# Optimization experiments

Measured on AMD Instinct MI355X. Metric: run time of the kernel, lower is better.

Reference implementation:

```python
import jax, jax.numpy as jnp
import numpy as np

N = 50000   # nodes
E = 800000  # edges (avg degree 16)
D = 128     # in_dim == out_dim
EPS = 1e-5  # LayerNorm eps (torch default)


def setup_inputs() -> dict:
    key = jax.random.key(0)
    ks = jax.random.split(key, 8)
    x = jax.random.normal(ks[0], (N, D), dtype=jnp.float32)
    edge_row = jax.random.randint(ks[1], (E,), 0, N, dtype=jnp.int32)
    edge_col = jax.random.randint(ks[2], (E,), 0, N, dtype=jnp.int32)
    edge_val = jax.random.uniform(ks[3], (E,), dtype=jnp.float32)
    W = jax.random.normal(ks[4], (D, D), dtype=jnp.float32) / np.sqrt(D).astype(np.float32)
    b = jnp.zeros((D,), jnp.float32)
    gamma = jnp.ones((D,), jnp.float32)
    beta = jnp.zeros((D,), jnp.float32)
    return {"x": x, "edge_val": edge_val, "W": W, "b": b,
            "gamma": gamma, "beta": beta,
            "edge_row": edge_row, "edge_col": edge_col}


def reference(x, edge_val, W, b, gamma, beta, edge_row, edge_col):
    # SpMM: support = adj @ x, adj in COO form (row, col, val)
    msgs = edge_val[:, None] * x[edge_col]                      # [E, D] gather
    support = jax.ops.segment_sum(msgs, edge_row, num_segments=x.shape[0])  # [N, D]
    # Linear (torch stores weight as [out, in])
    h = support @ W.T + b                                       # [N, D]
    # LayerNorm over last dim
    mu = jnp.mean(h, axis=-1, keepdims=True)
    var = jnp.mean(jnp.square(h - mu), axis=-1, keepdims=True)
    h = (h - mu) * jax.lax.rsqrt(var + EPS) * gamma + beta
    # ReLU; dropout is identity at inference
    return jax.nn.relu(h)
```

## Files before the change

### kernel.cpp

```cpp
#include <hip/hip_runtime.h>

#define D 128
#define LN_EPS 1e-5f
#define RPB 16
#define POISON 0xAAAAAAAAu
#define BINSTRIDE 4864
#define SBF_STRIDE 68
#define SH_STRIDE 132
#define ECAP 68
#define EMAX 64
#define P1BLOCKS 512
#define P1THREADS 1024
#define DENSECAP 1600
#define CURSTRIDE 16

typedef __attribute__((ext_vector_type(8))) short short8;
typedef __attribute__((ext_vector_type(4))) float f32x4;

union FragU { uint4 u; short8 s; };

__device__ __forceinline__ unsigned bf16_hi(float f) {
    unsigned u = __float_as_uint(f);
    return (u + 0x7FFFu + ((u >> 16) & 1u)) & 0xFFFF0000u;
}
__device__ __forceinline__ float lo16f(unsigned u) { return __uint_as_float(u << 16); }
__device__ __forceinline__ float hi16f(unsigned u) { return __uint_as_float(u & 0xFFFF0000u); }

__global__ void __launch_bounds__(P1THREADS) prep1_kernel(
    const int* __restrict__ edge_row, const int* __restrict__ edge_col,
    const float* __restrict__ edge_val,
    const float* __restrict__ W, const float* __restrict__ x,
    unsigned* __restrict__ Wb, unsigned* __restrict__ xb16,
    unsigned* __restrict__ bin_cursor, uint2* __restrict__ binbuf,
    int E, int n8, int nbins, int epb) {
    __shared__ int cntL[256];
    __shared__ int curL[256];
    __shared__ int lbaseL[256];
    __shared__ int gbaseL[256];
    __shared__ int tmp[2][256];
    __shared__ uint2 dense[DENSECAP];
    int t = threadIdx.x;
    int gid = blockIdx.x * P1THREADS + t;
    int gsz = gridDim.x * P1THREADS;

    if (t < 256) cntL[t] = 0;

    if (gid < 8192) {
        int u  = gid & 3;
        int L  = (gid >> 2) & 63;
        int nt = (gid >> 8) & 7;
        int kt = gid >> 11;
        int n = nt * 16 + (L & 15);
        int k = kt * 32 + (L >> 4) * 8 + u * 2;
        unsigned lo = bf16_hi(W[n * D + k]) >> 16;
        unsigned hi = bf16_hi(W[n * D + k + 1]);
        Wb[gid] = hi | lo;
    }

    for (int j = gid; j < n8; j += gsz) {
        float4 a = *(const float4*)(x + (size_t)j * 8);
        float4 c = *(const float4*)(x + (size_t)j * 8 + 4);
        uint4 o;
        o.x = bf16_hi(a.y) | (bf16_hi(a.x) >> 16);
        o.y = bf16_hi(a.w) | (bf16_hi(a.z) >> 16);
        o.z = bf16_hi(c.y) | (bf16_hi(c.x) >> 16);
        o.w = bf16_hi(c.w) | (bf16_hi(c.z) >> 16);
        *(uint4*)(xb16 + (size_t)j * 4) = o;
    }
    __syncthreads();

    int e0 = blockIdx.x * epb;
    int e1 = e0 + epb; if (e1 > E) e1 = E;
    int nume = e1 - e0; if (nume < 0) nume = 0;

    {
        int i = e0 + t * 4;
        for (; i + 3 < e1; i += P1THREADS * 4) {
            int4 r = *(const int4*)(edge_row + i);
            atomicAdd(&cntL[r.x >> 8], 1);
            atomicAdd(&cntL[r.y >> 8], 1);
            atomicAdd(&cntL[r.z >> 8], 1);
            atomicAdd(&cntL[r.w >> 8], 1);
        }
        for (; i < e1; ++i) atomicAdd(&cntL[edge_row[i] >> 8], 1);
    }
    __syncthreads();

    if (t < nbins) {
        int c = cntL[t];
        gbaseL[t] = c ? (int)(atomicAdd(&bin_cursor[t * CURSTRIDE], (unsigned)c) - POISON) : 0;
    }
    if (t < 256) tmp[0][t] = cntL[t];
    __syncthreads();
    int buf = 0;
    for (int off = 1; off < 256; off <<= 1) {
        if (t < 256) {
            int v = tmp[buf][t];
            if (t >= off) v += tmp[buf][t - off];
            tmp[1 - buf][t] = v;
        }
        buf ^= 1;
        __syncthreads();
    }
    if (t < 256) {
        lbaseL[t] = tmp[buf][t] - cntL[t];
        curL[t] = 0;
    }
    __syncthreads();

    {
        int i = e0 + t * 4;
        for (; i + 3 < e1; i += P1THREADS * 4) {
            int4 r = *(const int4*)(edge_row + i);
            int4 c = *(const int4*)(edge_col + i);
            float4 v = *(const float4*)(edge_val + i);
            int b0 = r.x >> 8, b1 = r.y >> 8, b2 = r.z >> 8, b3 = r.w >> 8;
            int p0 = atomicAdd(&curL[b0], 1) + lbaseL[b0];
            int p1 = atomicAdd(&curL[b1], 1) + lbaseL[b1];
            int p2 = atomicAdd(&curL[b2], 1) + lbaseL[b2];
            int p3 = atomicAdd(&curL[b3], 1) + lbaseL[b3];
            dense[p0] = make_uint2(((unsigned)c.x << 16) | (unsigned)(r.x & 255),
                                   bf16_hi(v.x) | (unsigned)b0);
            dense[p1] = make_uint2(((unsigned)c.y << 16) | (unsigned)(r.y & 255),
                                   bf16_hi(v.y) | (unsigned)b1);
            dense[p2] = make_uint2(((unsigned)c.z << 16) | (unsigned)(r.z & 255),
                                   bf16_hi(v.z) | (unsigned)b2);
            dense[p3] = make_uint2(((unsigned)c.w << 16) | (unsigned)(r.w & 255),
                                   bf16_hi(v.w) | (unsigned)b3);
        }
        for (; i < e1; ++i) {
            int r = edge_row[i];
            int bin = r >> 8;
            int p = atomicAdd(&curL[bin], 1) + lbaseL[bin];
            dense[p] = make_uint2(((unsigned)edge_col[i] << 16) | (unsigned)(r & 255),
                                  bf16_hi(edge_val[i]) | (unsigned)bin);
        }
    }
    __syncthreads();

    for (int i = t; i < nume; i += P1THREADS) {
        uint2 rec = dense[i];
        int bin = (int)(rec.y & 255u);
        int pos = gbaseL[bin] + (i - lbaseL[bin]);
        if (pos < BINSTRIDE)
            binbuf[(size_t)bin * BINSTRIDE + pos] =
                make_uint2(rec.x, rec.y & 0xFFFF0000u);
    }
}

__global__ void __launch_bounds__(256) fused_gather_linear(
    const unsigned* __restrict__ xb16, const uint2* __restrict__ binbuf,
    const unsigned* __restrict__ bin_cursor, const unsigned* __restrict__ Wb,
    const float* __restrict__ b, const float* __restrict__ gamma,
    const float* __restrict__ beta, float* __restrict__ out, int N) {
    __shared__ unsigned ecol[RPB][ECAP];
    __shared__ int ecnt[RPB];
    __shared__ int pdeg[RPB];
    __shared__ unsigned sbf[RPB][SBF_STRIDE];
    __shared__ float sh[RPB][SH_STRIDE];
    __shared__ float mu_s[RPB], inv_s[RPB];
    int t = threadIdx.x;

    int nwg = (int)gridDim.x;
    int swq = nwg >> 3, swr = nwg & 7;
    int xcd = (int)blockIdx.x & 7;
    int logical = (xcd < swr ? xcd * (swq + 1) : swr * (swq + 1) + (xcd - swr) * swq)
                + ((int)blockIdx.x >> 3);
    int row0 = logical * RPB;
    int bin  = logical >> 4;
    int tb   = (logical & 15) * RPB;

    if (t < RPB) ecnt[t] = 0;
    int sz = (int)(bin_cursor[bin * CURSTRIDE] - POISON);
    if (sz > BINSTRIDE) sz = BINSTRIDE;
    if (sz < 0) sz = 0;
    const uint2* bb = binbuf + (size_t)bin * BINSTRIDE;
    __syncthreads();

    {
        int half = sz >> 1;
        for (int i = t; i < half; i += 256) {
            uint4 two = *(const uint4*)(bb + (size_t)2 * i);
            int rl0 = (int)(two.x & 255u) - tb;
            if ((unsigned)rl0 < RPB) {
                int p = atomicAdd(&ecnt[rl0], 1);
                if (p < EMAX) ecol[rl0][p] = two.y | (two.x >> 16);
            }
            int rl1 = (int)(two.z & 255u) - tb;
            if ((unsigned)rl1 < RPB) {
                int p = atomicAdd(&ecnt[rl1], 1);
                if (p < EMAX) ecol[rl1][p] = two.w | (two.z >> 16);
            }
        }
        if (t == 0 && (sz & 1)) {
            uint2 rec = bb[sz - 1];
            int rl = (int)(rec.x & 255u) - tb;
            if ((unsigned)rl < RPB) {
                int p = atomicAdd(&ecnt[rl], 1);
                if (p < EMAX) ecol[rl][p] = rec.y | (rec.x >> 16);
            }
        }
    }
    __syncthreads();
    if (t < RPB) {
        int c = ecnt[t]; if (c > EMAX) c = EMAX;
        int pe = (c + 3) & ~3;
        for (int k = c; k < pe; ++k) ecol[t][k] = 0;
        pdeg[t] = pe;
    }
    __syncthreads();

    {
        int r = t >> 4;
        int qd = t & 15;
        int row = row0 + r;
        float4 accA = make_float4(0.f, 0.f, 0.f, 0.f);
        float4 accB = make_float4(0.f, 0.f, 0.f, 0.f);
        if (row < N) {
            int pd = pdeg[r];
            const unsigned* xb = xb16 + qd * 4;
            if (pd > 0) {
                uint4 p = *(const uint4*)&ecol[r][0];
                uint4 X0 = *(const uint4*)(xb + (size_t)(p.x & 0xFFFFu) * (D / 2));
                uint4 X1 = *(const uint4*)(xb + (size_t)(p.y & 0xFFFFu) * (D / 2));
                uint4 X2 = *(const uint4*)(xb + (size_t)(p.z & 0xFFFFu) * (D / 2));
                uint4 X3 = *(const uint4*)(xb + (size_t)(p.w & 0xFFFFu) * (D / 2));
                for (int e = 4;; e += 4) {
                    uint4 pn, Y0, Y1, Y2, Y3;
                    bool more = e < pd;
                    if (more) {
                        pn = *(const uint4*)&ecol[r][e];
                        Y0 = *(const uint4*)(xb + (size_t)(pn.x & 0xFFFFu) * (D / 2));
                        Y1 = *(const uint4*)(xb + (size_t)(pn.y & 0xFFFFu) * (D / 2));
                        Y2 = *(const uint4*)(xb + (size_t)(pn.z & 0xFFFFu) * (D / 2));
                        Y3 = *(const uint4*)(xb + (size_t)(pn.w & 0xFFFFu) * (D / 2));
                    }
                    float w0 = __uint_as_float(p.x & 0xFFFF0000u);
                    float w1 = __uint_as_float(p.y & 0xFFFF0000u);
                    float w2 = __uint_as_float(p.z & 0xFFFF0000u);
                    float w3 = __uint_as_float(p.w & 0xFFFF0000u);
                    accA.x = fmaf(w0, lo16f(X0.x), accA.x);
                    accA.y = fmaf(w0, hi16f(X0.x), accA.y);
                    accA.z = fmaf(w0, lo16f(X0.y), accA.z);
                    accA.w = fmaf(w0, hi16f(X0.y), accA.w);
                    accB.x = fmaf(w0, lo16f(X0.z), accB.x);
                    accB.y = fmaf(w0, hi16f(X0.z), accB.y);
                    accB.z = fmaf(w0, lo16f(X0.w), accB.z);
                    accB.w = fmaf(w0, hi16f(X0.w), accB.w);
                    accA.x = fmaf(w1, lo16f(X1.x), accA.x);
                    accA.y = fmaf(w1, hi16f(X1.x), accA.y);
                    accA.z = fmaf(w1, lo16f(X1.y), accA.z);
                    accA.w = fmaf(w1, hi16f(X1.y), accA.w);
                    accB.x = fmaf(w1, lo16f(X1.z), accB.x);
                    accB.y = fmaf(w1, hi16f(X1.z), accB.y);
                    accB.z = fmaf(w1, lo16f(X1.w), accB.z);
                    accB.w = fmaf(w1, hi16f(X1.w), accB.w);
                    accA.x = fmaf(w2, lo16f(X2.x), accA.x);
                    accA.y = fmaf(w2, hi16f(X2.x), accA.y);
                    accA.z = fmaf(w2, lo16f(X2.y), accA.z);
                    accA.w = fmaf(w2, hi16f(X2.y), accA.w);
                    accB.x = fmaf(w2, lo16f(X2.z), accB.x);
                    accB.y = fmaf(w2, hi16f(X2.z), accB.y);
                    accB.z = fmaf(w2, lo16f(X2.w), accB.z);
                    accB.w = fmaf(w2, hi16f(X2.w), accB.w);
                    accA.x = fmaf(w3, lo16f(X3.x), accA.x);
                    accA.y = fmaf(w3, hi16f(X3.x), accA.y);
                    accA.z = fmaf(w3, lo16f(X3.y), accA.z);
                    accA.w = fmaf(w3, hi16f(X3.y), accA.w);
                    accB.x = fmaf(w3, lo16f(X3.z), accB.x);
                    accB.y = fmaf(w3, hi16f(X3.z), accB.y);
                    accB.z = fmaf(w3, lo16f(X3.w), accB.z);
                    accB.w = fmaf(w3, hi16f(X3.w), accB.w);
                    if (!more) break;
                    p = pn; X0 = Y0; X1 = Y1; X2 = Y2; X3 = Y3;
                }
            }
        }
        uint4 o;
        o.x = bf16_hi(accA.y) | (bf16_hi(accA.x) >> 16);
        o.y = bf16_hi(accA.w) | (bf16_hi(accA.z) >> 16);
        o.z = bf16_hi(accB.y) | (bf16_hi(accB.x) >> 16);
        o.w = bf16_hi(accB.w) | (bf16_hi(accB.z) >> 16);
        *(uint4*)&sbf[r][qd * 4] = o;
    }
    __syncthreads();

    {
        int L = t & 63;
        int w = t >> 6;
        int m = L & 15;
        int g = L >> 4;
        f32x4 acc0 = {0.f, 0.f, 0.f, 0.f};
        f32x4 acc1 = {0.f, 0.f, 0.f, 0.f};
#pragma unroll
        for (int kt = 0; kt < 4; ++kt) {
            FragU a, b0, b1;
            a.u  = *(const uint4*)&sbf[m][kt * 16 + g * 4];
            b0.u = *(const uint4*)(Wb + (((size_t)(kt * 8 + w * 2)) * 64 + L) * 4);
            b1.u = *(const uint4*)(Wb + (((size_t)(kt * 8 + w * 2 + 1)) * 64 + L) * 4);
            acc0 = __builtin_amdgcn_mfma_f32_16x16x32_bf16(a.s, b0.s, acc0, 0, 0, 0);
            acc1 = __builtin_amdgcn_mfma_f32_16x16x32_bf16(a.s, b1.s, acc1, 0, 0, 0);
        }
        int n0 = w * 32 + m;
        int n1 = n0 + 16;
        float bv0 = b[n0], bv1 = b[n1];
#pragma unroll
        for (int i = 0; i < 4; ++i) {
            int rr = g * 4 + i;
            sh[rr][n0] = acc0[i] + bv0;
            sh[rr][n1] = acc1[i] + bv1;
        }
    }
    __syncthreads();

    {
        int rr = t >> 4, j = t & 15;
        float sum = 0.f, sq = 0.f;
#pragma unroll
        for (int i = 0; i < 8; ++i) {
            float v = sh[rr][j + 16 * i];
            sum += v;
            sq = fmaf(v, v, sq);
        }
#pragma unroll
        for (int off = 8; off > 0; off >>= 1) {
            sum += __shfl_down(sum, off, 16);
            sq  += __shfl_down(sq, off, 16);
        }
        if (j == 0) {
            float mu = sum * (1.0f / D);
            float var = sq * (1.0f / D) - mu * mu;
            mu_s[rr] = mu;
            inv_s[rr] = rsqrtf(var + LN_EPS);
        }
    }
    __syncthreads();

    {
        int td = t & 127;
        int rbase = (t >> 7) * 8;
        float g = gamma[td], be = beta[td];
#pragma unroll
        for (int r = 0; r < 8; ++r) {
            int row = row0 + rbase + r;
            if (row < N) {
                float y = (sh[rbase + r][td] - mu_s[rbase + r]) * inv_s[rbase + r] * g + be;
                out[(size_t)row * D + td] = fmaxf(y, 0.f);
            }
        }
    }
}

extern "C" void kernel_launch(void* const* d_in, const int* in_sizes, int n_in,
                              void* d_out, int out_size, void* d_ws, size_t ws_size,
                              hipStream_t stream) {
    const float* x        = (const float*)d_in[0];
    const float* edge_val = (const float*)d_in[1];
    const float* W        = (const float*)d_in[2];
    const float* b        = (const float*)d_in[3];
    const float* gamma    = (const float*)d_in[4];
    const float* beta     = (const float*)d_in[5];
    const int*   edge_row = (const int*)d_in[6];
    const int*   edge_col = (const int*)d_in[7];

    const int N = in_sizes[0] / D;
    const int E = in_sizes[1];
    const int n8 = N * D / 8;
    const int nbins = (N + 255) >> 8;

    char* ws = (char*)d_ws;
    uint2*    binbuf     = (uint2*)ws;     ws += (size_t)nbins * BINSTRIDE * sizeof(uint2);
    unsigned* xb16       = (unsigned*)ws;  ws += (size_t)N * (D / 2) * sizeof(unsigned);
    unsigned* Wb         = (unsigned*)ws;  ws += 8192 * sizeof(unsigned);
    unsigned* bin_cursor = (unsigned*)ws;  ws += 256 * CURSTRIDE * sizeof(unsigned);

    int epb = ((E + P1BLOCKS - 1) / P1BLOCKS + 3) & ~3;

    prep1_kernel<<<P1BLOCKS, P1THREADS, 0, stream>>>(edge_row, edge_col, edge_val,
                                                     W, x, Wb, xb16, bin_cursor,
                                                     binbuf, E, n8, nbins, epb);
    fused_gather_linear<<<(N + RPB - 1) / RPB, 256, 0, stream>>>(
        xb16, binbuf, bin_cursor, Wb, b, gamma, beta, (float*)d_out, N);
}
```

Baseline: 147.7 us.

## Reorder linear before aggregation: precompute xW in prep, gather transformed rows

Uses associativity (A·X)·Wᵀ = A·(X·Wᵀ) to apply the linear layer to every node's features in the prep kernel with MFMA, storing bf16 results. The second kernel then only gathers and accumulates the transformed rows, adding bias and doing LayerNorm and ReLU in registers with shuffles. This drops the shared-memory staging and the per-tile GEMM from the critical kernel. In exchange the prep kernel does a dense GEMM over all nodes, needs about 40KB of extra shared memory (W held in LDS), and rounds the GEMM output to bf16 before aggregation, which changes numerics. The gather loop also loses its software prefetch.

```diff
diff --git a/kernel.cpp b/kernel.cpp
--- a/kernel.cpp
+++ b/kernel.cpp
@@ -5,8 +5,7 @@
 #define RPB 16
 #define POISON 0xAAAAAAAAu
 #define BINSTRIDE 4864
-#define SBF_STRIDE 68
-#define SH_STRIDE 132
+#define XST_STRIDE 68
 #define ECAP 68
 #define EMAX 64
 #define P1BLOCKS 512
@@ -30,9 +29,11 @@
     const int* __restrict__ edge_row, const int* __restrict__ edge_col,
     const float* __restrict__ edge_val,
     const float* __restrict__ W, const float* __restrict__ x,
-    unsigned* __restrict__ Wb, unsigned* __restrict__ xb16,
+    unsigned* __restrict__ yb16,
     unsigned* __restrict__ bin_cursor, uint2* __restrict__ binbuf,
-    int E, int n8, int nbins, int epb) {
+    int E, int N, int nbins, int epb) {
+    __shared__ unsigned wbL[8192];
+    __shared__ unsigned xst[4][RPB][XST_STRIDE];
     __shared__ int cntL[256];
     __shared__ int curL[256];
     __shared__ int lbaseL[256];
@@ -40,34 +41,79 @@
     __shared__ int tmp[2][256];
     __shared__ uint2 dense[DENSECAP];
     int t = threadIdx.x;
-    int gid = blockIdx.x * P1THREADS + t;
-    int gsz = gridDim.x * P1THREADS;
 
     if (t < 256) cntL[t] = 0;
 
-    if (gid < 8192) {
-        int u  = gid & 3;
-        int L  = (gid >> 2) & 63;
-        int nt = (gid >> 8) & 7;
-        int kt = gid >> 11;
+    for (int i = t; i < 8192; i += P1THREADS) {
+        int u  = i & 3;
+        int L  = (i >> 2) & 63;
+        int nt = (i >> 8) & 7;
+        int kt = i >> 11;
         int n = nt * 16 + (L & 15);
         int k = kt * 32 + (L >> 4) * 8 + u * 2;
         unsigned lo = bf16_hi(W[n * D + k]) >> 16;
         unsigned hi = bf16_hi(W[n * D + k + 1]);
-        Wb[gid] = hi | lo;
-    }
-
-    for (int j = gid; j < n8; j += gsz) {
-        float4 a = *(const float4*)(x + (size_t)j * 8);
-        float4 c = *(const float4*)(x + (size_t)j * 8 + 4);
-        uint4 o;
-        o.x = bf16_hi(a.y) | (bf16_hi(a.x) >> 16);
-        o.y = bf16_hi(a.w) | (bf16_hi(a.z) >> 16);
-        o.z = bf16_hi(c.y) | (bf16_hi(c.x) >> 16);
-        o.w = bf16_hi(c.w) | (bf16_hi(c.z) >> 16);
-        *(uint4*)(xb16 + (size_t)j * 4) = o;
-    }
-    __syncthreads();
+        wbL[i] = hi | lo;
+    }
+    __syncthreads();
+
+    {
+        int T = (N + RPB - 1) / RPB;
+        int g = t >> 8;
+        int tg = t & 255;
+        for (int tb0 = blockIdx.x * 4; tb0 < T; tb0 += gridDim.x * 4) {
+            int tile = tb0 + g;
+            if (tile < T) {
+                int r = tg >> 4, q = tg & 15;
+                int row = tile * RPB + r;
+                uint4 o = make_uint4(0u, 0u, 0u, 0u);
+                if (row < N) {
+                    float4 a = *(const float4*)(x + (size_t)row * D + q * 8);
+                    float4 c = *(const float4*)(x + (size_t)row * D + q * 8 + 4);
+                    o.x = bf16_hi(a.y) | (bf16_hi(a.x) >> 16);
+                    o.y = bf16_hi(a.w) | (bf16_hi(a.z) >> 16);
+                    o.z = bf16_hi(c.y) | (bf16_hi(c.x) >> 16);
+                    o.w = bf16_hi(c.w) | (bf16_hi(c.z) >> 16);
+                }
+                *(uint4*)&xst[g][r][q * 4] = o;
+            }
+            __syncthreads();
+            if (tile < T) {
+                int L = tg & 63;
+                int w = tg >> 6;
+                int m = L & 15;
+                int gk = L >> 4;
+                f32x4 acc0 = {0.f, 0.f, 0.f, 0.f};
+                f32x4 acc1 = {0.f, 0.f, 0.f, 0.f};
+#pragma unroll
+                for (int kt = 0; kt < 4; ++kt) {
+                    FragU a, b0, b1;
+                    a.u  = *(const uint4*)&xst[g][m][kt * 16 + gk * 4];
+                    b0.u = *(const uint4*)(wbL + (((size_t)(kt * 8 + w * 2)) * 64 + L) * 4);
+                    b1.u = *(const uint4*)(wbL + (((size_t)(kt * 8 + w * 2 + 1)) * 64 + L) * 4);
+                    acc0 = __builtin_amdgcn_mfma_f32_16x16x32_bf16(a.s, b0.s, acc0, 0, 0, 0);
+                    acc1 = __builtin_amdgcn_mfma_f32_16x16x32_bf16(a.s, b1.s, acc1, 0, 0, 0);
+                }
+                bool evenm = (m & 1) == 0;
+#pragma unroll
+                for (int i = 0; i < 4; ++i) {
+                    float p0 = __shfl_xor(acc0[i], 1);
+                    float p1 = __shfl_xor(acc1[i], 1);
+                    if (evenm) {
+                        int row = tile * RPB + gk * 4 + i;
+                        if (row < N) {
+                            unsigned y0 = bf16_hi(p0) | (bf16_hi(acc0[i]) >> 16);
+                            unsigned y1 = bf16_hi(p1) | (bf16_hi(acc1[i]) >> 16);
+                            size_t base = (size_t)row * (D / 2) + w * 16 + (m >> 1);
+                            yb16[base] = y0;
+                            yb16[base + 8] = y1;
+                        }
+                    }
+                }
+            }
+            __syncthreads();
+        }
+    }
 
     int e0 = blockIdx.x * epb;
     int e1 = e0 + epb; if (e1 > E) e1 = E;
@@ -148,17 +194,14 @@
     }
 }
 
-__global__ void __launch_bounds__(256) fused_gather_linear(
-    const unsigned* __restrict__ xb16, const uint2* __restrict__ binbuf,
-    const unsigned* __restrict__ bin_cursor, const unsigned* __restrict__ Wb,
-    const float* __restrict__ b, const float* __restrict__ gamma,
+__global__ void __launch_bounds__(256) fused_lite(
+    const unsigned* __restrict__ yb16, const uint2* __restrict__ binbuf,
+    const unsigned* __restrict__ bin_cursor,
+    const float* __restrict__ bias, const float* __restrict__ gamma,
     const float* __restrict__ beta, float* __restrict__ out, int N) {
     __shared__ unsigned ecol[RPB][ECAP];
     __shared__ int ecnt[RPB];
     __shared__ int pdeg[RPB];
-    __shared__ unsigned sbf[RPB][SBF_STRIDE];
-    __shared__ float sh[RPB][SH_STRIDE];
-    __shared__ float mu_s[RPB], inv_s[RPB];
     int t = threadIdx.x;
 
     int nwg = (int)gridDim.x;
@@ -218,135 +261,93 @@
         float4 accB = make_float4(0.f, 0.f, 0.f, 0.f);
         if (row < N) {
             int pd = pdeg[r];
-            const unsigned* xb = xb16 + qd * 4;
-            if (pd > 0) {
-                uint4 p = *(const uint4*)&ecol[r][0];
-                uint4 X0 = *(const uint4*)(xb + (size_t)(p.x & 0xFFFFu) * (D / 2));
-                uint4 X1 = *(const uint4*)(xb + (size_t)(p.y & 0xFFFFu) * (D / 2));
-                uint4 X2 = *(const uint4*)(xb + (size_t)(p.z & 0xFFFFu) * (D / 2));
-                uint4 X3 = *(const uint4*)(xb + (size_t)(p.w & 0xFFFFu) * (D / 2));
-                for (int e = 4;; e += 4) {
-                    uint4 pn, Y0, Y1, Y2, Y3;
-                    bool more = e < pd;
-                    if (more) {
-                        pn = *(const uint4*)&ecol[r][e];
-                        Y0 = *(const uint4*)(xb + (size_t)(pn.x & 0xFFFFu) * (D / 2));
-                        Y1 = *(const uint4*)(xb + (size_t)(pn.y & 0xFFFFu) * (D / 2));
-                        Y2 = *(const uint4*)(xb + (size_t)(pn.z & 0xFFFFu) * (D / 2));
-                        Y3 = *(const uint4*)(xb + (size_t)(pn.w & 0xFFFFu) * (D / 2));
-                    }
-                    float w0 = __uint_as_float(p.x & 0xFFFF0000u);
-                    float w1 = __uint_as_float(p.y & 0xFFFF0000u);
-                    float w2 = __uint_as_float(p.z & 0xFFFF0000u);
-                    float w3 = __uint_as_float(p.w & 0xFFFF0000u);
-                    accA.x = fmaf(w0, lo16f(X0.x), accA.x);
-                    accA.y = fmaf(w0, hi16f(X0.x), accA.y);
-                    accA.z = fmaf(w0, lo16f(X0.y), accA.z);
-                    accA.w = fmaf(w0, hi16f(X0.y), accA.w);
-                    accB.x = fmaf(w0, lo16f(X0.z), accB.x);
-                    accB.y = fmaf(w0, hi16f(X0.z), accB.y);
-                    accB.z = fmaf(w0, lo16f(X0.w), accB.z);
-                    accB.w = fmaf(w0, hi16f(X0.w), accB.w);
-                    accA.x = fmaf(w1, lo16f(X1.x), accA.x);
-                    accA.y = fmaf(w1, hi16f(X1.x), accA.y);
-                    accA.z = fmaf(w1, lo16f(X1.y), accA.z);
-                    accA.w = fmaf(w1, hi16f(X1.y), accA.w);
-                    accB.x = fmaf(w1, lo16f(X1.z), accB.x);
-                    accB.y = fmaf(w1, hi16f(X1.z), accB.y);
-                    accB.z = fmaf(w1, lo16f(X1.w), accB.z);
-                    accB.w = fmaf(w1, hi16f(X1.w), accB.w);
-                    accA.x = fmaf(w2, lo16f(X2.x), accA.x);
-                    accA.y = fmaf(w2, hi16f(X2.x), accA.y);
-                    accA.z = fmaf(w2, lo16f(X2.y), accA.z);
-                    accA.w = fmaf(w2, hi16f(X2.y), accA.w);
-                    accB.x = fmaf(w2, lo16f(X2.z), accB.x);
-                    accB.y = fmaf(w2, hi16f(X2.z), accB.y);
-                    accB.z = fmaf(w2, lo16f(X2.w), accB.z);
-                    accB.w = fmaf(w2, hi16f(X2.w), accB.w);
-                    accA.x = fmaf(w3, lo16f(X3.x), accA.x);
-                    accA.y = fmaf(w3, hi16f(X3.x), accA.y);
-                    accA.z = fmaf(w3, lo16f(X3.y), accA.z);
-                    accA.w = fmaf(w3, hi16f(X3.y), accA.w);
-                    accB.x = fmaf(w3, lo16f(X3.z), accB.x);
-                    accB.y = fmaf(w3, hi16f(X3.z), accB.y);
-                    accB.z = fmaf(w3, lo16f(X3.w), accB.z);
-                    accB.w = fmaf(w3, hi16f(X3.w), accB.w);
-                    if (!more) break;
-                    p = pn; X0 = Y0; X1 = Y1; X2 = Y2; X3 = Y3;
-                }
-            }
-        }
-        uint4 o;
-        o.x = bf16_hi(accA.y) | (bf16_hi(accA.x) >> 16);
-        o.y = bf16_hi(accA.w) | (bf16_hi(accA.z) >> 16);
-        o.z = bf16_hi(accB.y) | (bf16_hi(accB.x) >> 16);
-        o.w = bf16_hi(accB.w) | (bf16_hi(accB.z) >> 16);
-        *(uint4*)&sbf[r][qd * 4] = o;
-    }
-    __syncthreads();
-
-    {
-        int L = t & 63;
-        int w = t >> 6;
-        int m = L & 15;
-        int g = L >> 4;
-        f32x4 acc0 = {0.f, 0.f, 0.f, 0.f};
-        f32x4 acc1 = {0.f, 0.f, 0.f, 0.f};
-#pragma unroll
-        for (int kt = 0; kt < 4; ++kt) {
-            FragU a, b0, b1;
-            a.u  = *(const uint4*)&sbf[m][kt * 16 + g * 4];
-            b0.u = *(const uint4*)(Wb + (((size_t)(kt * 8 + w * 2)) * 64 + L) * 4);
-            b1.u = *(const uint4*)(Wb + (((size_t)(kt * 8 + w * 2 + 1)) * 64 + L) * 4);
-            acc0 = __builtin_amdgcn_mfma_f32_16x16x32_bf16(a.s, b0.s, acc0, 0, 0, 0);
-            acc1 = __builtin_amdgcn_mfma_f32_16x16x32_bf16(a.s, b1.s, acc1, 0, 0, 0);
-        }
-        int n0 = w * 32 + m;
-        int n1 = n0 + 16;
-        float bv0 = b[n0], bv1 = b[n1];
-#pragma unroll
-        for (int i = 0; i < 4; ++i) {
-            int rr = g * 4 + i;
-            sh[rr][n0] = acc0[i] + bv0;
-            sh[rr][n1] = acc1[i] + bv1;
-        }
-    }
-    __syncthreads();
-
-    {
-        int rr = t >> 4, j = t & 15;
-        float sum = 0.f, sq = 0.f;
-#pragma unroll
-        for (int i = 0; i < 8; ++i) {
-            float v = sh[rr][j + 16 * i];
-            sum += v;
-            sq = fmaf(v, v, sq);
-        }
+            const unsigned* yb = yb16 + qd * 4;
+            for (int e = 0; e < pd; e += 4) {
+                uint4 p = *(const uint4*)&ecol[r][e];
+                unsigned c0 = p.x & 0xFFFFu, c1 = p.y & 0xFFFFu;
+                unsigned c2 = p.z & 0xFFFFu, c3 = p.w & 0xFFFFu;
+                float w0 = __uint_as_float(p.x & 0xFFFF0000u);
+                float w1 = __uint_as_float(p.y & 0xFFFF0000u);
+                float w2 = __uint_as_float(p.z & 0xFFFF0000u);
+                float w3 = __uint_as_float(p.w & 0xFFFF0000u);
+                uint4 X0 = *(const uint4*)(yb + (size_t)c0 * (D / 2));
+                uint4 X1 = *(const uint4*)(yb + (size_t)c1 * (D / 2));
+                uint4 X2 = *(const uint4*)(yb + (size_t)c2 * (D / 2));
+                uint4 X3 = *(const uint4*)(yb + (size_t)c3 * (D / 2));
+                accA.x = fmaf(w0, lo16f(X0.x), accA.x);
+                accA.y = fmaf(w0, hi16f(X0.x), accA.y);
+                accA.z = fmaf(w0, lo16f(X0.y), accA.z);
+                accA.w = fmaf(w0, hi16f(X0.y), accA.w);
+                accB.x = fmaf(w0, lo16f(X0.z), accB.x);
+                accB.y = fmaf(w0, hi16f(X0.z), accB.y);
+                accB.z = fmaf(w0, lo16f(X0.w), accB.z);
+                accB.w = fmaf(w0, hi16f(X0.w), accB.w);
+                accA.x = fmaf(w1, lo16f(X1.x), accA.x);
+                accA.y = fmaf(w1, hi16f(X1.x), accA.y);
+                accA.z = fmaf(w1, lo16f(X1.y), accA.z);
+                accA.w = fmaf(w1, hi16f(X1.y), accA.w);
+                accB.x = fmaf(w1, lo16f(X1.z), accB.x);
+                accB.y = fmaf(w1, hi16f(X1.z), accB.y);
+                accB.z = fmaf(w1, lo16f(X1.w), accB.z);
+                accB.w = fmaf(w1, hi16f(X1.w), accB.w);
+                accA.x = fmaf(w2, lo16f(X2.x), accA.x);
+                accA.y = fmaf(w2, hi16f(X2.x), accA.y);
+                accA.z = fmaf(w2, lo16f(X2.y), accA.z);
+                accA.w = fmaf(w2, hi16f(X2.y), accA.w);
+                accB.x = fmaf(w2, lo16f(X2.z), accB.x);
+                accB.y = fmaf(w2, hi16f(X2.z), accB.y);
+                accB.z = fmaf(w2, lo16f(X2.w), accB.z);
+                accB.w = fmaf(w2, hi16f(X2.w), accB.w);
+                accA.x = fmaf(w3, lo16f(X3.x), accA.x);
+                accA.y = fmaf(w3, hi16f(X3.x), accA.y);
+                accA.z = fmaf(w3, lo16f(X3.y), accA.z);
+                accA.w = fmaf(w3, hi16f(X3.y), accA.w);
+                accB.x = fmaf(w3, lo16f(X3.z), accB.x);
+                accB.y = fmaf(w3, hi16f(X3.z), accB.y);
+                accB.z = fmaf(w3, lo16f(X3.w), accB.z);
+                accB.w = fmaf(w3, hi16f(X3.w), accB.w);
+            }
+        }
+        float4 bA = *(const float4*)(bias + qd * 8);
+        float4 bB = *(const float4*)(bias + qd * 8 + 4);
+        accA.x += bA.x; accA.y += bA.y; accA.z += bA.z; accA.w += bA.w;
+        accB.x += bB.x; accB.y += bB.y; accB.z += bB.z; accB.w += bB.w;
+
+        float sum = accA.x + accA.y + accA.z + accA.w
+                  + accB.x + accB.y + accB.z + accB.w;
+        float sq = accA.x * accA.x;
+        sq = fmaf(accA.y, accA.y, sq);
+        sq = fmaf(accA.z, accA.z, sq);
+        sq = fmaf(accA.w, accA.w, sq);
+        sq = fmaf(accB.x, accB.x, sq);
+        sq = fmaf(accB.y, accB.y, sq);
+        sq = fmaf(accB.z, accB.z, sq);
+        sq = fmaf(accB.w, accB.w, sq);
 #pragma unroll
         for (int off = 8; off > 0; off >>= 1) {
-            sum += __shfl_down(sum, off, 16);
-            sq  += __shfl_down(sq, off, 16);
-        }
-        if (j == 0) {
-            float mu = sum * (1.0f / D);
-            float var = sq * (1.0f / D) - mu * mu;
-            mu_s[rr] = mu;
-            inv_s[rr] = rsqrtf(var + LN_EPS);
-        }
-    }
-    __syncthreads();
-
-    {
-        int td = t & 127;
-        int rbase = (t >> 7) * 8;
-        float g = gamma[td], be = beta[td];
-#pragma unroll
-        for (int r = 0; r < 8; ++r) {
-            int row = row0 + rbase + r;
-            if (row < N) {
-                float y = (sh[rbase + r][td] - mu_s[rbase + r]) * inv_s[rbase + r] * g + be;
-                out[(size_t)row * D + td] = fmaxf(y, 0.f);
-            }
+            sum += __shfl_xor(sum, off, 16);
+            sq  += __shfl_xor(sq, off, 16);
+        }
+        float mu = sum * (1.0f / D);
+        float var = sq * (1.0f / D) - mu * mu;
+        float inv = rsqrtf(var + LN_EPS);
+
+        if (row < N) {
+            float4 gA = *(const float4*)(gamma + qd * 8);
+            float4 gB = *(const float4*)(gamma + qd * 8 + 4);
+            float4 eA = *(const float4*)(beta + qd * 8);
+            float4 eB = *(const float4*)(beta + qd * 8 + 4);
+            float4 oA, oB;
+            oA.x = fmaxf((accA.x - mu) * inv * gA.x + eA.x, 0.f);
+            oA.y = fmaxf((accA.y - mu) * inv * gA.y + eA.y, 0.f);
+            oA.z = fmaxf((accA.z - mu) * inv * gA.z + eA.z, 0.f);
+            oA.w = fmaxf((accA.w - mu) * inv * gA.w + eA.w, 0.f);
+            oB.x = fmaxf((accB.x - mu) * inv * gB.x + eB.x, 0.f);
+            oB.y = fmaxf((accB.y - mu) * inv * gB.y + eB.y, 0.f);
+            oB.z = fmaxf((accB.z - mu) * inv * gB.z + eB.z, 0.f);
+            oB.w = fmaxf((accB.w - mu) * inv * gB.w + eB.w, 0.f);
+            *(float4*)(out + (size_t)row * D + qd * 8) = oA;
+            *(float4*)(out + (size_t)row * D + qd * 8 + 4) = oB;
         }
     }
 }
@@ -365,20 +366,18 @@
 
     const int N = in_sizes[0] / D;
     const int E = in_sizes[1];
-    const int n8 = N * D / 8;
     const int nbins = (N + 255) >> 8;
 
     char* ws = (char*)d_ws;
     uint2*    binbuf     = (uint2*)ws;     ws += (size_t)nbins * BINSTRIDE * sizeof(uint2);
-    unsigned* xb16       = (unsigned*)ws;  ws += (size_t)N * (D / 2) * sizeof(unsigned);
-    unsigned* Wb         = (unsigned*)ws;  ws += 8192 * sizeof(unsigned);
+    unsigned* yb16       = (unsigned*)ws;  ws += (size_t)N * (D / 2) * sizeof(unsigned);
     unsigned* bin_cursor = (unsigned*)ws;  ws += 256 * CURSTRIDE * sizeof(unsigned);
 
     int epb = ((E + P1BLOCKS - 1) / P1BLOCKS + 3) & ~3;
 
     prep1_kernel<<<P1BLOCKS, P1THREADS, 0, stream>>>(edge_row, edge_col, edge_val,
-                                                     W, x, Wb, xb16, bin_cursor,
-                                                     binbuf, E, n8, nbins, epb);
-    fused_gather_linear<<<(N + RPB - 1) / RPB, 256, 0, stream>>>(
-        xb16, binbuf, bin_cursor, Wb, b, gamma, beta, (float*)d_out, N);
+                                                     W, x, yb16, bin_cursor,
+                                                     binbuf, E, N, nbins, epb);
+    fused_lite<<<(N + RPB - 1) / RPB, 256, 0, stream>>>(
+        yb16, binbuf, bin_cursor, b, gamma, beta, (float*)d_out, N);
 }
```

Measured after the change: 146.0 us. No clear change (-1.1%).
